# Kernel optimization log

Measured on AMD Instinct MI355X. Metric: run time of the kernel, lower is better.

## Reference

```python
import jax, jax.numpy as jnp
import numpy as np

N_NODES = 50000
N_EDGES = 800000
IN_CH = 64
HID = 128
N_LAYERS = 4
LN_EPS = 1e-5


def setup_inputs() -> dict:
    key = jax.random.key(0)
    ks = jax.random.split(key, 10)
    x = jax.random.normal(ks[0], (N_NODES, IN_CH), dtype=jnp.float32)
    edge_index = jax.random.randint(ks[1], (2, N_EDGES), 0, N_NODES, dtype=jnp.int64)
    edge_weight = jax.random.uniform(ks[2], (N_EDGES,), dtype=jnp.float32)
    # parameters
    W_in = jax.random.normal(ks[3], (IN_CH, HID), dtype=jnp.float32) / np.sqrt(IN_CH)
    b_in = jnp.zeros((HID,), dtype=jnp.float32)
    conv_W = jax.random.normal(ks[4], (N_LAYERS, HID, HID), dtype=jnp.float32) / np.sqrt(HID)
    conv_b = jnp.zeros((N_LAYERS, HID), dtype=jnp.float32)
    ln_g = jnp.ones((N_LAYERS, HID), dtype=jnp.float32)
    ln_b = jnp.zeros((N_LAYERS, HID), dtype=jnp.float32)
    return {"x": x, "edge_index": edge_index, "edge_weight": edge_weight,
            "W_in": W_in, "b_in": b_in, "conv_W": conv_W, "conv_b": conv_b,
            "ln_g": ln_g, "ln_b": ln_b}


def _layer_norm(h, g, b):
    mu = jnp.mean(h, axis=-1, keepdims=True)
    var = jnp.mean((h - mu) ** 2, axis=-1, keepdims=True)
    return (h - mu) * jax.lax.rsqrt(var + LN_EPS) * g + b


def reference(x, edge_index, edge_weight, W_in, b_in, conv_W, conv_b, ln_g, ln_b):
    N = x.shape[0]
    # input projection + relu (dropout is identity at eval)
    h = jax.nn.relu(x @ W_in + b_in)

    # GCN normalization with self-loops (PyG GCNConv semantics, fill_value=1)
    src = edge_index[0]
    dst = edge_index[1]
    loop = jnp.arange(N, dtype=src.dtype)
    src_f = jnp.concatenate([src, loop])            # [E+N]
    dst_f = jnp.concatenate([dst, loop])
    w_f = jnp.concatenate([edge_weight, jnp.ones((N,), dtype=edge_weight.dtype)])
    deg = jax.ops.segment_sum(w_f, dst_f, num_segments=N)
    dinv = jnp.where(deg > 0, jax.lax.rsqrt(jnp.maximum(deg, 1e-30)), 0.0)
    norm = dinv[src_f] * w_f * dinv[dst_f]          # [E+N]

    for l in range(N_LAYERS):
        residual = h
        m = h @ conv_W[l]                           # [N, HID]
        # gather messages over edges, scale, scatter-add to targets
        agg = jax.ops.segment_sum(m[src_f] * norm[:, None], dst_f, num_segments=N)
        agg = agg + conv_b[l]
        h = jax.nn.relu(_layer_norm(agg, ln_g[l], ln_b[l])) + residual
    return h
```

## Files before the change

kernel.cpp:

```cpp
#include <hip/hip_runtime.h>
#include <hip/hip_bf16.h>

#define NN 50000
#define NE 800000
#define IN_CH 64
#define HID 128
#define NL 4
#define LN_EPS 1e-5f

#define ECAP 1150000
#define WSCALE 1048576.0f
#define VSCALE 32767.0f

typedef __attribute__((ext_vector_type(8))) short s8v;
typedef __attribute__((ext_vector_type(4))) float f4v;

__device__ inline ushort f2bf(float x) {
    __hip_bfloat16 h = __float2bfloat16(x);
    return *(ushort*)&h;
}
__device__ inline float4 i8u(uint u) {
    float4 r;
    r.x = (float)(int)(signed char)(u & 0xffu);
    r.y = (float)(int)(signed char)((u >> 8) & 0xffu);
    r.z = (float)(int)(signed char)((u >> 16) & 0xffu);
    r.w = (float)(int)(signed char)(u >> 24);
    return r;
}


__global__ void k_zero(int4* __restrict__ p, int n4) {
    int i = blockIdx.x * blockDim.x + threadIdx.x;
    if (i < n4) p[i] = make_int4(0, 0, 0, 0);
}

__global__ void k_deg_cnt(const int* __restrict__ ei, const float* __restrict__ ew,
                          unsigned long long* __restrict__ pk, int* __restrict__ ord) {
    int e = blockIdx.x * blockDim.x + threadIdx.x;
    if (e >= NE) return;
    int d = ei[NE + e];
    unsigned int wq = (unsigned int)__float2uint_rn(ew[e] * WSCALE);
    unsigned long long old = atomicAdd(&pk[d], (1ULL << 32) | (unsigned long long)wq);
    ord[e] = (int)(old >> 32);
}

__global__ __launch_bounds__(1024) void k_scan_a(const unsigned long long* __restrict__ pk,
                                                 int* __restrict__ rowp_tmp,
                                                 int* __restrict__ bsum,
                                                 float* __restrict__ dinv) {
    __shared__ int wsum[16];
    int tid = threadIdx.x;
    int lane = tid & 63, wv = tid >> 6;
    int i = blockIdx.x * 1024 + tid;
    unsigned long long pv = (i < NN) ? pk[i] : 0ULL;
    if (i < NN) {
        float deg = (float)(unsigned int)(pv & 0xffffffffu) * (1.0f / WSCALE);
        dinv[i] = rsqrtf(deg + 1.0f);
    }
    int v = (((int)(pv >> 32) + 7) & ~7);
    int s = v;
#pragma unroll
    for (int off = 1; off < 64; off <<= 1) {
        int t = __shfl_up(s, off, 64);
        if (lane >= off) s += t;
    }
    if (lane == 63) wsum[wv] = s;
    __syncthreads();
    int woff = 0;
    for (int w = 0; w < wv; w++) woff += wsum[w];
    if (i < NN) rowp_tmp[i] = woff + s - v;
    if (tid == 1023) bsum[blockIdx.x] = woff + s;
}

__global__ __launch_bounds__(64) void k_scan_b(const int* __restrict__ bsum,
                                               int* __restrict__ boff,
                                               int* __restrict__ rowp, int nb) {
    int t = threadIdx.x;
    int v = (t < nb) ? bsum[t] : 0;
    int s = v;
#pragma unroll
    for (int off = 1; off < 64; off <<= 1) {
        int u = __shfl_up(s, off, 64);
        if (t >= off) s += u;
    }
    if (t < nb) boff[t] = s - v;
    if (t == 63) rowp[NN] = s;
}

__global__ __launch_bounds__(1024) void k_scan_c(const int* __restrict__ rowp_tmp,
                                                 const int* __restrict__ boff,
                                                 const unsigned long long* __restrict__ pk,
                                                 int* __restrict__ rowp,
                                                 uint* __restrict__ erec) {
    int i = blockIdx.x * 1024 + threadIdx.x;
    if (i >= NN) return;
    int start = rowp_tmp[i] + boff[blockIdx.x];
    rowp[i] = start;
    int cnt = (int)(pk[i] >> 32);
    int v = (cnt + 7) & ~7;
    for (int p = start + cnt; p < start + v; p++) erec[p] = 0u;
}

__global__ void k_scatter(const int* __restrict__ ei, const float* __restrict__ ew,
                          const float* __restrict__ dinv, const int* __restrict__ rowp,
                          const int* __restrict__ ord, uint* __restrict__ erec) {
    int e = blockIdx.x * blockDim.x + threadIdx.x;
    if (e >= NE) return;
    int s = ei[e];
    int d = ei[NE + e];
    int pos = rowp[d] + ord[e];
    float v = dinv[s] * ew[e] * dinv[d];
    uint q = (uint)__float2int_rn(v * VSCALE);
    erec[pos] = ((uint)s << 15) | q;
}

__global__ __launch_bounds__(256) void k_wpack(const float* __restrict__ cW,
                                               ushort* __restrict__ Wp) {
    int gid = blockIdx.x * 256 + threadIdx.x;
    int lane = gid & 63;
    int t = (gid >> 6) & 7;
    int kc = (gid >> 9) & 3;
    int layer = gid >> 11;
    const float* W = cW + (size_t)layer * HID * HID;
    int kbase = kc * 32 + (lane >> 4) * 8;
    int col = t * 16 + (lane & 15);
    ushort o[8];
#pragma unroll
    for (int j = 0; j < 8; j++) o[j] = f2bf(W[(size_t)(kbase + j) * HID + col]);
    uint4 pk4;
    pk4.x = (uint)o[0] | ((uint)o[1] << 16);
    pk4.y = (uint)o[2] | ((uint)o[3] << 16);
    pk4.z = (uint)o[4] | ((uint)o[5] << 16);
    pk4.w = (uint)o[6] | ((uint)o[7] << 16);
    ((uint4*)Wp)[gid] = pk4;
}

__global__ __launch_bounds__(256) void k_inproj(const float* __restrict__ x,
                                                const float* __restrict__ W,
                                                const float* __restrict__ b,
                                                float* __restrict__ h) {
    __shared__ float xs[64][IN_CH];
    int tid = threadIdx.x;
    int cx = tid & 31;
    int ny = tid >> 5;
    int nbase = blockIdx.x * 64;
    const float4* xg = (const float4*)(x + (size_t)nbase * IN_CH);
    float4* xs4 = (float4*)xs;
#pragma unroll
    for (int p = 0; p < 4; p++) {
        int i = p * 256 + tid;
        int row = i >> 4;
        xs4[i] = (nbase + row < NN) ? xg[i] : make_float4(0, 0, 0, 0);
    }
    __syncthreads();
    float4 acc[8];
#pragma unroll
    for (int j = 0; j < 8; j++) acc[j] = make_float4(0, 0, 0, 0);
    const float4* W4 = (const float4*)W;
#pragma unroll 4
    for (int k4 = 0; k4 < IN_CH / 4; k4++) {
        int k = 4 * k4;
        float4 w0 = W4[(k + 0) * 32 + cx];
        float4 w1 = W4[(k + 1) * 32 + cx];
        float4 w2 = W4[(k + 2) * 32 + cx];
        float4 w3 = W4[(k + 3) * 32 + cx];
#pragma unroll
        for (int j = 0; j < 8; j++) {
            float4 hv = *(const float4*)&xs[ny * 8 + j][k];
            acc[j].x += hv.x * w0.x + hv.y * w1.x + hv.z * w2.x + hv.w * w3.x;
            acc[j].y += hv.x * w0.y + hv.y * w1.y + hv.z * w2.y + hv.w * w3.y;
            acc[j].z += hv.x * w0.z + hv.y * w1.z + hv.z * w2.z + hv.w * w3.z;
            acc[j].w += hv.x * w0.w + hv.y * w1.w + hv.z * w2.w + hv.w * w3.w;
        }
    }
    float4 bc = ((const float4*)b)[cx];
    float4* mg = (float4*)h;
#pragma unroll
    for (int j = 0; j < 8; j++) {
        int n = nbase + ny * 8 + j;
        if (n < NN) {
            float4 o;
            o.x = fmaxf(acc[j].x + bc.x, 0.f);
            o.y = fmaxf(acc[j].y + bc.y, 0.f);
            o.z = fmaxf(acc[j].z + bc.z, 0.f);
            o.w = fmaxf(acc[j].w + bc.w, 0.f);
            mg[n * 32 + cx] = o;
        }
    }
}

__global__ __launch_bounds__(256) void k_gemm(const float* __restrict__ h,
                                              const ushort* __restrict__ Wp,
                                              signed char* __restrict__ m8,
                                              float* __restrict__ sc) {
    int tid = threadIdx.x;
    int w = tid >> 6, l = tid & 63;
    int q = l >> 4, r16 = l & 15;
    int rowbase = blockIdx.x * 64 + w * 16;
    f4v acc[8];
#pragma unroll
    for (int t = 0; t < 8; t++) acc[t] = (f4v){0.f, 0.f, 0.f, 0.f};
    const s8v* wp = (const s8v*)Wp;
    int row = rowbase + r16;
#pragma unroll
    for (int kc = 0; kc < 4; kc++) {
        s8v afrag;
        if (row < NN) {
            const float4* hp = (const float4*)(h + (size_t)row * HID + kc * 32 + q * 8);
            float4 h0 = hp[0], h1 = hp[1];
            afrag[0] = (short)f2bf(h0.x); afrag[1] = (short)f2bf(h0.y);
            afrag[2] = (short)f2bf(h0.z); afrag[3] = (short)f2bf(h0.w);
            afrag[4] = (short)f2bf(h1.x); afrag[5] = (short)f2bf(h1.y);
            afrag[6] = (short)f2bf(h1.z); afrag[7] = (short)f2bf(h1.w);
        } else {
            afrag = (s8v){0, 0, 0, 0, 0, 0, 0, 0};
        }
#pragma unroll
        for (int t = 0; t < 8; t++) {
            s8v bfrag = wp[(kc * 8 + t) * 64 + l];
            acc[t] = __builtin_amdgcn_mfma_f32_16x16x32_bf16(afrag, bfrag, acc[t], 0, 0, 0);
        }
    }
#pragma unroll
    for (int rg = 0; rg < 4; rg++) {
        float rmax = 0.f;
#pragma unroll
        for (int t = 0; t < 8; t++) rmax = fmaxf(rmax, fabsf(acc[t][rg]));
#pragma unroll
        for (int off = 1; off < 16; off <<= 1)
            rmax = fmaxf(rmax, __shfl_xor(rmax, off, 16));
        rmax = fmaxf(rmax, 1e-20f);
        float scale = rmax * (1.0f / 127.0f);
        float inv = 127.0f / rmax;
        int orow = rowbase + q * 4 + rg;
        if (orow < NN) {
#pragma unroll
            for (int t = 0; t < 8; t++) {
                int qi = __float2int_rn(acc[t][rg] * inv);
                m8[(size_t)orow * HID + t * 16 + r16] = (signed char)qi;
            }
            if (r16 == 0) sc[orow] = scale;
        }
    }
}

__global__ __launch_bounds__(256) void k_agg(const signed char* __restrict__ m8,
                                             const float* __restrict__ sc,
                                             const int* __restrict__ rowp,
                                             const uint* __restrict__ erec,
                                             const float* __restrict__ dinv,
                                             const float* __restrict__ cb,
                                             const float* __restrict__ g,
                                             const float* __restrict__ bb,
                                             float* __restrict__ h) {
    int lane = threadIdx.x & 63;
    int sub = lane & 31;
    int hi = lane >> 5;
    int n = blockIdx.x * 4 + (threadIdx.x >> 6);
    if (n >= NN) return;
    const uint* mu = (const uint*)m8;
    float dn = dinv[n];
    float selfs = hi ? 0.0f : dn * dn * sc[n];
    float4 sv = i8u(mu[(size_t)n * 32 + sub]);
    float4 a0, a1, a2, a3;
    a0.x = selfs * sv.x; a0.y = selfs * sv.y; a0.z = selfs * sv.z; a0.w = selfs * sv.w;
    a1 = make_float4(0, 0, 0, 0);
    a2 = make_float4(0, 0, 0, 0);
    a3 = make_float4(0, 0, 0, 0);
    int r0 = rowp[n], r1 = rowp[n + 1];
    const uint4* e4 = (const uint4*)erec;
    for (int r = r0; r < r1; r += 8) {
        int qb = r >> 2;
        uint4 rA = e4[qb + 0];
        uint4 rB = e4[qb + 1];
        uint c0 = hi ? rA.y : rA.x;
        uint c1 = hi ? rA.w : rA.z;
        uint c2 = hi ? rB.y : rB.x;
        uint c3 = hi ? rB.w : rB.z;
        int s0 = c0 >> 15;  int s1 = c1 >> 15;
        int s2 = c2 >> 15;  int s3 = c3 >> 15;
        float v0 = (float)(c0 & 32767u) * (1.0f / VSCALE) * sc[s0];
        float v1 = (float)(c1 & 32767u) * (1.0f / VSCALE) * sc[s1];
        float v2 = (float)(c2 & 32767u) * (1.0f / VSCALE) * sc[s2];
        float v3 = (float)(c3 & 32767u) * (1.0f / VSCALE) * sc[s3];
        float4 f0 = i8u(mu[(size_t)s0 * 32 + sub]);
        float4 f1 = i8u(mu[(size_t)s1 * 32 + sub]);
        float4 f2 = i8u(mu[(size_t)s2 * 32 + sub]);
        float4 f3 = i8u(mu[(size_t)s3 * 32 + sub]);
        a0.x += v0 * f0.x; a0.y += v0 * f0.y; a0.z += v0 * f0.z; a0.w += v0 * f0.w;
        a1.x += v1 * f1.x; a1.y += v1 * f1.y; a1.z += v1 * f1.z; a1.w += v1 * f1.w;
        a2.x += v2 * f2.x; a2.y += v2 * f2.y; a2.z += v2 * f2.z; a2.w += v2 * f2.w;
        a3.x += v3 * f3.x; a3.y += v3 * f3.y; a3.z += v3 * f3.z; a3.w += v3 * f3.w;
    }
    float4 acc;
    acc.x = a0.x + a1.x + a2.x + a3.x;
    acc.y = a0.y + a1.y + a2.y + a3.y;
    acc.z = a0.z + a1.z + a2.z + a3.z;
    acc.w = a0.w + a1.w + a2.w + a3.w;
    acc.x += __shfl_xor(acc.x, 32, 64);
    acc.y += __shfl_xor(acc.y, 32, 64);
    acc.z += __shfl_xor(acc.z, 32, 64);
    acc.w += __shfl_xor(acc.w, 32, 64);
    float4 cbv = ((const float4*)cb)[sub];
    acc.x += cbv.x; acc.y += cbv.y; acc.z += cbv.z; acc.w += cbv.w;
    float s1 = acc.x + acc.y + acc.z + acc.w;
    float s2 = acc.x * acc.x + acc.y * acc.y + acc.z * acc.z + acc.w * acc.w;
#pragma unroll
    for (int off = 16; off > 0; off >>= 1) {
        s1 += __shfl_down(s1, off, 32);
        s2 += __shfl_down(s2, off, 32);
    }
    s1 = __shfl(s1, 0, 32);
    s2 = __shfl(s2, 0, 32);
    float mu_ = s1 * (1.0f / HID);
    float var = s2 * (1.0f / HID) - mu_ * mu_;
    float rs = rsqrtf(var + LN_EPS);
    if (hi == 0) {
        float4 gv = ((const float4*)g)[sub];
        float4 bv = ((const float4*)bb)[sub];
        float4* h4 = (float4*)h;
        float4 hv = h4[(size_t)n * 32 + sub];
        float4 o;
        o.x = fmaxf((acc.x - mu_) * rs * gv.x + bv.x, 0.f) + hv.x;
        o.y = fmaxf((acc.y - mu_) * rs * gv.y + bv.y, 0.f) + hv.y;
        o.z = fmaxf((acc.z - mu_) * rs * gv.z + bv.z, 0.f) + hv.z;
        o.w = fmaxf((acc.w - mu_) * rs * gv.w + bv.w, 0.f) + hv.w;
        h4[(size_t)n * 32 + sub] = o;
    }
}


extern "C" void kernel_launch(void* const* d_in, const int* in_sizes, int n_in,
                              void* d_out, int out_size, void* d_ws, size_t ws_size,
                              hipStream_t stream) {
    const float* x    = (const float*)d_in[0];
    const int*   ei   = (const int*)d_in[1];
    const float* ew   = (const float*)d_in[2];
    const float* W_in = (const float*)d_in[3];
    const float* b_in = (const float*)d_in[4];
    const float* cW   = (const float*)d_in[5];
    const float* cb   = (const float*)d_in[6];
    const float* lg   = (const float*)d_in[7];
    const float* lb   = (const float*)d_in[8];
    float* h = (float*)d_out;

    char* ws = (char*)d_ws;
    unsigned long long* pk = (unsigned long long*)(ws + 0);
    int*    rowp     = (int*)   (ws + 401408);
    int*    rowp_tmp = (int*)   (ws + 602112);
    int*    bsum     = (int*)   (ws + 802816);
    int*    boff     = (int*)   (ws + 803072);
    uint*   erec     = (uint*)  (ws + 803328);
    float*  dinv     = (float*) (ws + 5403328);
    ushort* Wp       = (ushort*)(ws + 5603328);
    signed char* m8  = (signed char*)(ws + 5734400);
    int*    ord      = (int*)   (ws + 5734400);
    float*  sc       = (float*) (ws + 12134400);

    const int NB = (NN + 1023) / 1024;

    k_zero<<<(100000 / 4 + 255) / 256, 256, 0, stream>>>((int4*)pk, 100000 / 4);
    k_deg_cnt<<<(NE + 255) / 256, 256, 0, stream>>>(ei, ew, pk, ord);
    k_scan_a<<<NB, 1024, 0, stream>>>(pk, rowp_tmp, bsum, dinv);
    k_scan_b<<<1, 64, 0, stream>>>(bsum, boff, rowp, NB);
    k_scan_c<<<NB, 1024, 0, stream>>>(rowp_tmp, boff, pk, rowp, erec);
    k_scatter<<<(NE + 255) / 256, 256, 0, stream>>>(ei, ew, dinv, rowp, ord, erec);
    k_wpack<<<32, 256, 0, stream>>>(cW, Wp);

    k_inproj<<<(NN + 63) / 64, 256, 0, stream>>>(x, W_in, b_in, h);

    for (int l = 0; l < NL; l++) {
        k_gemm<<<(NN + 63) / 64, 256, 0, stream>>>(h, Wp + (size_t)l * 16384, m8, sc);
        k_agg<<<(NN + 3) / 4, 256, 0, stream>>>(m8, sc, rowp, erec, dinv,
                                                cb + l * HID, lg + l * HID, lb + l * HID, h);
    }
}
```

Measured before the change: 277.8 us.

## Merge independent preprocessing kernels into block-partitioned combined launches

Folds the degree count, input projection and weight packing into a single launch whose blocks are split by index range. It also merges the edge scatter with the first layer's GEMM, which lets the first aggregation follow directly. The `ord` buffer moves out of the region it shared with `m8`, because the layer-0 GEMM now writes `m8` while the scatter still reads `ord`. The aim is to cut kernel launch count and fill the GPU better with independent small stages, at the cost of mixed block types and the shared-memory footprint applying to every block.

After: 268.3 us. 1.04x faster.

```diff
diff --git a/kernel.cpp b/kernel.cpp
--- a/kernel.cpp
+++ b/kernel.cpp
@@ -11,6 +11,12 @@
 #define ECAP 1150000
 #define WSCALE 1048576.0f
 #define VSCALE 32767.0f
+
+#define NB_DEG  3125
+#define NB_INP  782
+#define NB_WP   32
+#define NB_SCAT 3125
+#define NB_GEMM 782
 
 typedef __attribute__((ext_vector_type(8))) short s8v;
 typedef __attribute__((ext_vector_type(4))) float f4v;
@@ -29,19 +35,207 @@
 }
 
 
-__global__ void k_zero(int4* __restrict__ p, int n4) {
-    int i = blockIdx.x * blockDim.x + threadIdx.x;
-    if (i < n4) p[i] = make_int4(0, 0, 0, 0);
-}
-
-__global__ void k_deg_cnt(const int* __restrict__ ei, const float* __restrict__ ew,
-                          unsigned long long* __restrict__ pk, int* __restrict__ ord) {
-    int e = blockIdx.x * blockDim.x + threadIdx.x;
+__device__ inline void do_deg(int blk, const int* __restrict__ ei,
+                              const float* __restrict__ ew,
+                              unsigned long long* __restrict__ pk,
+                              int* __restrict__ ord) {
+    int e = blk * 256 + threadIdx.x;
     if (e >= NE) return;
     int d = ei[NE + e];
     unsigned int wq = (unsigned int)__float2uint_rn(ew[e] * WSCALE);
     unsigned long long old = atomicAdd(&pk[d], (1ULL << 32) | (unsigned long long)wq);
     ord[e] = (int)(old >> 32);
+}
+
+__device__ inline void do_inproj(int blk, const float* __restrict__ x,
+                                 const float* __restrict__ W,
+                                 const float* __restrict__ b,
+                                 float* __restrict__ h) {
+    __shared__ float xs[64][IN_CH];
+    int tid = threadIdx.x;
+    int cx = tid & 31;
+    int ny = tid >> 5;
+    int nbase = blk * 64;
+    const float4* xg = (const float4*)(x + (size_t)nbase * IN_CH);
+    float4* xs4 = (float4*)xs;
+#pragma unroll
+    for (int p = 0; p < 4; p++) {
+        int i = p * 256 + tid;
+        int row = i >> 4;
+        xs4[i] = (nbase + row < NN) ? xg[i] : make_float4(0, 0, 0, 0);
+    }
+    __syncthreads();
+    float4 acc[8];
+#pragma unroll
+    for (int j = 0; j < 8; j++) acc[j] = make_float4(0, 0, 0, 0);
+    const float4* W4 = (const float4*)W;
+#pragma unroll 4
+    for (int k4 = 0; k4 < IN_CH / 4; k4++) {
+        int k = 4 * k4;
+        float4 w0 = W4[(k + 0) * 32 + cx];
+        float4 w1 = W4[(k + 1) * 32 + cx];
+        float4 w2 = W4[(k + 2) * 32 + cx];
+        float4 w3 = W4[(k + 3) * 32 + cx];
+#pragma unroll
+        for (int j = 0; j < 8; j++) {
+            float4 hv = *(const float4*)&xs[ny * 8 + j][k];
+            acc[j].x += hv.x * w0.x + hv.y * w1.x + hv.z * w2.x + hv.w * w3.x;
+            acc[j].y += hv.x * w0.y + hv.y * w1.y + hv.z * w2.y + hv.w * w3.y;
+            acc[j].z += hv.x * w0.z + hv.y * w1.z + hv.z * w2.z + hv.w * w3.z;
+            acc[j].w += hv.x * w0.w + hv.y * w1.w + hv.z * w2.w + hv.w * w3.w;
+        }
+    }
+    float4 bc = ((const float4*)b)[cx];
+    float4* mg = (float4*)h;
+#pragma unroll
+    for (int j = 0; j < 8; j++) {
+        int n = nbase + ny * 8 + j;
+        if (n < NN) {
+            float4 o;
+            o.x = fmaxf(acc[j].x + bc.x, 0.f);
+            o.y = fmaxf(acc[j].y + bc.y, 0.f);
+            o.z = fmaxf(acc[j].z + bc.z, 0.f);
+            o.w = fmaxf(acc[j].w + bc.w, 0.f);
+            mg[n * 32 + cx] = o;
+        }
+    }
+}
+
+__device__ inline void do_wpack(int blk, const float* __restrict__ cW,
+                                ushort* __restrict__ Wp) {
+    int gid = blk * 256 + threadIdx.x;
+    int lane = gid & 63;
+    int t = (gid >> 6) & 7;
+    int kc = (gid >> 9) & 3;
+    int layer = gid >> 11;
+    const float* W = cW + (size_t)layer * HID * HID;
+    int kbase = kc * 32 + (lane >> 4) * 8;
+    int col = t * 16 + (lane & 15);
+    ushort o[8];
+#pragma unroll
+    for (int j = 0; j < 8; j++) o[j] = f2bf(W[(size_t)(kbase + j) * HID + col]);
+    uint4 pk4;
+    pk4.x = (uint)o[0] | ((uint)o[1] << 16);
+    pk4.y = (uint)o[2] | ((uint)o[3] << 16);
+    pk4.z = (uint)o[4] | ((uint)o[5] << 16);
+    pk4.w = (uint)o[6] | ((uint)o[7] << 16);
+    ((uint4*)Wp)[gid] = pk4;
+}
+
+__device__ inline void do_scatter(int blk, const int* __restrict__ ei,
+                                  const float* __restrict__ ew,
+                                  const float* __restrict__ dinv,
+                                  const int* __restrict__ rowp,
+                                  const int* __restrict__ ord,
+                                  uint* __restrict__ erec) {
+    int e = blk * 256 + threadIdx.x;
+    if (e >= NE) return;
+    int s = ei[e];
+    int d = ei[NE + e];
+    int pos = rowp[d] + ord[e];
+    float v = dinv[s] * ew[e] * dinv[d];
+    uint q = (uint)__float2int_rn(v * VSCALE);
+    erec[pos] = ((uint)s << 15) | q;
+}
+
+__device__ inline void do_gemm(int blk, const float* __restrict__ h,
+                               const ushort* __restrict__ Wp,
+                               signed char* __restrict__ m8,
+                               float* __restrict__ sc) {
+    int tid = threadIdx.x;
+    int w = tid >> 6, l = tid & 63;
+    int q = l >> 4, r16 = l & 15;
+    int rowbase = blk * 64 + w * 16;
+    f4v acc[8];
+#pragma unroll
+    for (int t = 0; t < 8; t++) acc[t] = (f4v){0.f, 0.f, 0.f, 0.f};
+    const s8v* wp = (const s8v*)Wp;
+    int row = rowbase + r16;
+#pragma unroll
+    for (int kc = 0; kc < 4; kc++) {
+        s8v afrag;
+        if (row < NN) {
+            const float4* hp = (const float4*)(h + (size_t)row * HID + kc * 32 + q * 8);
+            float4 h0 = hp[0], h1 = hp[1];
+            afrag[0] = (short)f2bf(h0.x); afrag[1] = (short)f2bf(h0.y);
+            afrag[2] = (short)f2bf(h0.z); afrag[3] = (short)f2bf(h0.w);
+            afrag[4] = (short)f2bf(h1.x); afrag[5] = (short)f2bf(h1.y);
+            afrag[6] = (short)f2bf(h1.z); afrag[7] = (short)f2bf(h1.w);
+        } else {
+            afrag = (s8v){0, 0, 0, 0, 0, 0, 0, 0};
+        }
+#pragma unroll
+        for (int t = 0; t < 8; t++) {
+            s8v bfrag = wp[(kc * 8 + t) * 64 + l];
+            acc[t] = __builtin_amdgcn_mfma_f32_16x16x32_bf16(afrag, bfrag, acc[t], 0, 0, 0);
+        }
+    }
+#pragma unroll
+    for (int rg = 0; rg < 4; rg++) {
+        float rmax = 0.f;
+#pragma unroll
+        for (int t = 0; t < 8; t++) rmax = fmaxf(rmax, fabsf(acc[t][rg]));
+#pragma unroll
+        for (int off = 1; off < 16; off <<= 1)
+            rmax = fmaxf(rmax, __shfl_xor(rmax, off, 16));
+        rmax = fmaxf(rmax, 1e-20f);
+        float scale = rmax * (1.0f / 127.0f);
+        float inv = 127.0f / rmax;
+        int orow = rowbase + q * 4 + rg;
+        if (orow < NN) {
+#pragma unroll
+            for (int t = 0; t < 8; t++) {
+                int qi = __float2int_rn(acc[t][rg] * inv);
+                m8[(size_t)orow * HID + t * 16 + r16] = (signed char)qi;
+            }
+            if (r16 == 0) sc[orow] = scale;
+        }
+    }
+}
+
+
+__global__ __launch_bounds__(256) void k_pre(const int* __restrict__ ei,
+                                             const float* __restrict__ ew,
+                                             unsigned long long* __restrict__ pk,
+                                             int* __restrict__ ord,
+                                             const float* __restrict__ x,
+                                             const float* __restrict__ W_in,
+                                             const float* __restrict__ b_in,
+                                             float* __restrict__ h,
+                                             const float* __restrict__ cW,
+                                             ushort* __restrict__ Wp) {
+    int b = blockIdx.x;
+    if (b < NB_DEG) {
+        do_deg(b, ei, ew, pk, ord);
+    } else if (b < NB_DEG + NB_INP) {
+        do_inproj(b - NB_DEG, x, W_in, b_in, h);
+    } else {
+        do_wpack(b - NB_DEG - NB_INP, cW, Wp);
+    }
+}
+
+__global__ __launch_bounds__(256) void k_scat_gemm(const int* __restrict__ ei,
+                                                   const float* __restrict__ ew,
+                                                   const float* __restrict__ dinv,
+                                                   const int* __restrict__ rowp,
+                                                   const int* __restrict__ ord,
+                                                   uint* __restrict__ erec,
+                                                   const float* __restrict__ h,
+                                                   const ushort* __restrict__ Wp,
+                                                   signed char* __restrict__ m8,
+                                                   float* __restrict__ sc) {
+    int b = blockIdx.x;
+    if (b < NB_SCAT) {
+        do_scatter(b, ei, ew, dinv, rowp, ord, erec);
+    } else {
+        do_gemm(b - NB_SCAT, h, Wp, m8, sc);
+    }
+}
+
+
+__global__ void k_zero(int4* __restrict__ p, int n4) {
+    int i = blockIdx.x * blockDim.x + threadIdx.x;
+    if (i < n4) p[i] = make_int4(0, 0, 0, 0);
 }
 
 __global__ __launch_bounds__(1024) void k_scan_a(const unsigned long long* __restrict__ pk,
@@ -101,147 +295,11 @@
     for (int p = start + cnt; p < start + v; p++) erec[p] = 0u;
 }
 
-__global__ void k_scatter(const int* __restrict__ ei, const float* __restrict__ ew,
-                          const float* __restrict__ dinv, const int* __restrict__ rowp,
-                          const int* __restrict__ ord, uint* __restrict__ erec) {
-    int e = blockIdx.x * blockDim.x + threadIdx.x;
-    if (e >= NE) return;
-    int s = ei[e];
-    int d = ei[NE + e];
-    int pos = rowp[d] + ord[e];
-    float v = dinv[s] * ew[e] * dinv[d];
-    uint q = (uint)__float2int_rn(v * VSCALE);
-    erec[pos] = ((uint)s << 15) | q;
-}
-
-__global__ __launch_bounds__(256) void k_wpack(const float* __restrict__ cW,
-                                               ushort* __restrict__ Wp) {
-    int gid = blockIdx.x * 256 + threadIdx.x;
-    int lane = gid & 63;
-    int t = (gid >> 6) & 7;
-    int kc = (gid >> 9) & 3;
-    int layer = gid >> 11;
-    const float* W = cW + (size_t)layer * HID * HID;
-    int kbase = kc * 32 + (lane >> 4) * 8;
-    int col = t * 16 + (lane & 15);
-    ushort o[8];
-#pragma unroll
-    for (int j = 0; j < 8; j++) o[j] = f2bf(W[(size_t)(kbase + j) * HID + col]);
-    uint4 pk4;
-    pk4.x = (uint)o[0] | ((uint)o[1] << 16);
-    pk4.y = (uint)o[2] | ((uint)o[3] << 16);
-    pk4.z = (uint)o[4] | ((uint)o[5] << 16);
-    pk4.w = (uint)o[6] | ((uint)o[7] << 16);
-    ((uint4*)Wp)[gid] = pk4;
-}
-
-__global__ __launch_bounds__(256) void k_inproj(const float* __restrict__ x,
-                                                const float* __restrict__ W,
-                                                const float* __restrict__ b,
-                                                float* __restrict__ h) {
-    __shared__ float xs[64][IN_CH];
-    int tid = threadIdx.x;
-    int cx = tid & 31;
-    int ny = tid >> 5;
-    int nbase = blockIdx.x * 64;
-    const float4* xg = (const float4*)(x + (size_t)nbase * IN_CH);
-    float4* xs4 = (float4*)xs;
-#pragma unroll
-    for (int p = 0; p < 4; p++) {
-        int i = p * 256 + tid;
-        int row = i >> 4;
-        xs4[i] = (nbase + row < NN) ? xg[i] : make_float4(0, 0, 0, 0);
-    }
-    __syncthreads();
-    float4 acc[8];
-#pragma unroll
-    for (int j = 0; j < 8; j++) acc[j] = make_float4(0, 0, 0, 0);
-    const float4* W4 = (const float4*)W;
-#pragma unroll 4
-    for (int k4 = 0; k4 < IN_CH / 4; k4++) {
-        int k = 4 * k4;
-        float4 w0 = W4[(k + 0) * 32 + cx];
-        float4 w1 = W4[(k + 1) * 32 + cx];
-        float4 w2 = W4[(k + 2) * 32 + cx];
-        float4 w3 = W4[(k + 3) * 32 + cx];
-#pragma unroll
-        for (int j = 0; j < 8; j++) {
-            float4 hv = *(const float4*)&xs[ny * 8 + j][k];
-            acc[j].x += hv.x * w0.x + hv.y * w1.x + hv.z * w2.x + hv.w * w3.x;
-            acc[j].y += hv.x * w0.y + hv.y * w1.y + hv.z * w2.y + hv.w * w3.y;
-            acc[j].z += hv.x * w0.z + hv.y * w1.z + hv.z * w2.z + hv.w * w3.z;
-            acc[j].w += hv.x * w0.w + hv.y * w1.w + hv.z * w2.w + hv.w * w3.w;
-        }
-    }
-    float4 bc = ((const float4*)b)[cx];
-    float4* mg = (float4*)h;
-#pragma unroll
-    for (int j = 0; j < 8; j++) {
-        int n = nbase + ny * 8 + j;
-        if (n < NN) {
-            float4 o;
-            o.x = fmaxf(acc[j].x + bc.x, 0.f);
-            o.y = fmaxf(acc[j].y + bc.y, 0.f);
-            o.z = fmaxf(acc[j].z + bc.z, 0.f);
-            o.w = fmaxf(acc[j].w + bc.w, 0.f);
-            mg[n * 32 + cx] = o;
-        }
-    }
-}
-
 __global__ __launch_bounds__(256) void k_gemm(const float* __restrict__ h,
                                               const ushort* __restrict__ Wp,
                                               signed char* __restrict__ m8,
                                               float* __restrict__ sc) {
-    int tid = threadIdx.x;
-    int w = tid >> 6, l = tid & 63;
-    int q = l >> 4, r16 = l & 15;
-    int rowbase = blockIdx.x * 64 + w * 16;
-    f4v acc[8];
-#pragma unroll
-    for (int t = 0; t < 8; t++) acc[t] = (f4v){0.f, 0.f, 0.f, 0.f};
-    const s8v* wp = (const s8v*)Wp;
-    int row = rowbase + r16;
-#pragma unroll
-    for (int kc = 0; kc < 4; kc++) {
-        s8v afrag;
-        if (row < NN) {
-            const float4* hp = (const float4*)(h + (size_t)row * HID + kc * 32 + q * 8);
-            float4 h0 = hp[0], h1 = hp[1];
-            afrag[0] = (short)f2bf(h0.x); afrag[1] = (short)f2bf(h0.y);
-            afrag[2] = (short)f2bf(h0.z); afrag[3] = (short)f2bf(h0.w);
-            afrag[4] = (short)f2bf(h1.x); afrag[5] = (short)f2bf(h1.y);
-            afrag[6] = (short)f2bf(h1.z); afrag[7] = (short)f2bf(h1.w);
-        } else {
-            afrag = (s8v){0, 0, 0, 0, 0, 0, 0, 0};
-        }
-#pragma unroll
-        for (int t = 0; t < 8; t++) {
-            s8v bfrag = wp[(kc * 8 + t) * 64 + l];
-            acc[t] = __builtin_amdgcn_mfma_f32_16x16x32_bf16(afrag, bfrag, acc[t], 0, 0, 0);
-        }
-    }
-#pragma unroll
-    for (int rg = 0; rg < 4; rg++) {
-        float rmax = 0.f;
-#pragma unroll
-        for (int t = 0; t < 8; t++) rmax = fmaxf(rmax, fabsf(acc[t][rg]));
-#pragma unroll
-        for (int off = 1; off < 16; off <<= 1)
-            rmax = fmaxf(rmax, __shfl_xor(rmax, off, 16));
-        rmax = fmaxf(rmax, 1e-20f);
-        float scale = rmax * (1.0f / 127.0f);
-        float inv = 127.0f / rmax;
-        int orow = rowbase + q * 4 + rg;
-        if (orow < NN) {
-#pragma unroll
-            for (int t = 0; t < 8; t++) {
-                int qi = __float2int_rn(acc[t][rg] * inv);
-                m8[(size_t)orow * HID + t * 16 + r16] = (signed char)qi;
-            }
-            if (r16 == 0) sc[orow] = scale;
-        }
-    }
+    do_gemm(blockIdx.x, h, Wp, m8, sc);
 }
 
 __global__ __launch_bounds__(256) void k_agg(const signed char* __restrict__ m8,
@@ -354,23 +412,24 @@
     float*  dinv     = (float*) (ws + 5403328);
     ushort* Wp       = (ushort*)(ws + 5603328);
     signed char* m8  = (signed char*)(ws + 5734400);
-    int*    ord      = (int*)   (ws + 5734400);
     float*  sc       = (float*) (ws + 12134400);
+    int*    ord      = (int*)   (ws + 12334400);
 
     const int NB = (NN + 1023) / 1024;
 
     k_zero<<<(100000 / 4 + 255) / 256, 256, 0, stream>>>((int4*)pk, 100000 / 4);
-    k_deg_cnt<<<(NE + 255) / 256, 256, 0, stream>>>(ei, ew, pk, ord);
+    k_pre<<<NB_DEG + NB_INP + NB_WP, 256, 0, stream>>>(ei, ew, pk, ord,
+                                                       x, W_in, b_in, h, cW, Wp);
     k_scan_a<<<NB, 1024, 0, stream>>>(pk, rowp_tmp, bsum, dinv);
     k_scan_b<<<1, 64, 0, stream>>>(bsum, boff, rowp, NB);
     k_scan_c<<<NB, 1024, 0, stream>>>(rowp_tmp, boff, pk, rowp, erec);
-    k_scatter<<<(NE + 255) / 256, 256, 0, stream>>>(ei, ew, dinv, rowp, ord, erec);
-    k_wpack<<<32, 256, 0, stream>>>(cW, Wp);
-
-    k_inproj<<<(NN + 63) / 64, 256, 0, stream>>>(x, W_in, b_in, h);
-
-    for (int l = 0; l < NL; l++) {
-        k_gemm<<<(NN + 63) / 64, 256, 0, stream>>>(h, Wp + (size_t)l * 16384, m8, sc);
+    k_scat_gemm<<<NB_SCAT + NB_GEMM, 256, 0, stream>>>(ei, ew, dinv, rowp, ord, erec,
+                                                       h, Wp, m8, sc);
+
+    k_agg<<<(NN + 3) / 4, 256, 0, stream>>>(m8, sc, rowp, erec, dinv,
+                                            cb, lg, lb, h);
+    for (int l = 1; l < NL; l++) {
+        k_gemm<<<NB_GEMM, 256, 0, stream>>>(h, Wp + (size_t)l * 16384, m8, sc);
         k_agg<<<(NN + 3) / 4, 256, 0, stream>>>(m8, sc, rowp, erec, dinv,
                                                 cb + l * HID, lg + l * HID, lb + l * HID, h);
     }
```
